# Performance work log

Measured on AMD Instinct MI355X. Metric: run time of the kernel, lower is better.

The kernel has to match this reference:

```python
import math
import jax, jax.numpy as jnp
import numpy as np

B, QC, KC, RES, SRC = 4, 512, 256, 64, 128
T = RES * RES


def setup_inputs():
    key = jax.random.key(0)
    ks = jax.random.split(key, 8)
    return {
        "key_feat": jax.random.normal(ks[0], (B, KC, SRC, SRC), jnp.float32),
        "query": jax.random.normal(ks[1], (B, QC, RES, RES), jnp.float32),
        "Weight_Mat": jax.random.uniform(ks[2], (B, T, T), dtype=jnp.float32),
        "key_proj_w": jax.random.normal(ks[3], (QC, KC), jnp.float32) * 0.02,
        "norm_w": jnp.ones((QC,), jnp.float32),
        "norm_b": jnp.zeros((QC,), jnp.float32),
        "qkv_w": jax.random.normal(ks[4], (3 * QC, 2 * QC), jnp.float32) * 0.02,
        "qkv_b": jax.random.normal(ks[5], (3 * QC,), jnp.float32) * 0.02,
        "proj_w": jax.random.normal(ks[6], (QC, QC), jnp.float32) * 0.02,
        "proj_b": jnp.zeros((QC,), jnp.float32),
    }


def group_norm(x, w, b, groups=32, eps=1e-5):
    # x: (b, C, L) -- GroupNorm over channel groups and spatial dim
    bs, C, L = x.shape
    xg = x.reshape(bs, groups, C // groups, L)
    mu = xg.mean(axis=(2, 3), keepdims=True)
    var = xg.var(axis=(2, 3), keepdims=True)
    xn = ((xg - mu) * jax.lax.rsqrt(var + eps)).reshape(bs, C, L)
    return xn * w[None, :, None] + b[None, :, None]


def reference(key_feat, query, Weight_Mat, key_proj_w, norm_w, norm_b, qkv_w, qkv_b, proj_w, proj_b):
    b, qc, H, W = query.shape
    f = key_feat.shape[2] // H  # exact integer downsample factor (2)
    # F.interpolate bilinear (align_corners=False) at exact 1/f rate == f x f average pooling
    kds = key_feat.reshape(b, key_feat.shape[1], H, f, W, f).mean(axis=(3, 5))
    # Weight_Mat interpolate has scale==1 in source (no-op), elided.
    k = jnp.einsum('oc,bchw->bohw', key_proj_w, kds).reshape(b, qc, H * W)
    q = query.reshape(b, qc, H * W)
    q = group_norm(q, norm_w, norm_b)
    k = group_norm(k, norm_w, norm_b)
    # qkv: 1x1 conv1d on concat(q, k) -> (b, 3*qc, T)
    qkv = jnp.einsum('oc,bct->bot', qkv_w, jnp.concatenate([q, k], axis=1)) + qkv_b[None, :, None]
    qq, kk, vv = jnp.split(qkv, 3, axis=1)  # each (b, qc, T); num_heads=1 so ch=qc
    scale = qc ** -0.25  # 1/sqrt(sqrt(ch))
    logits = Weight_Mat * jnp.einsum('bct,bcs->bts', qq * scale, kk * scale)
    attn = jax.nn.softmax(logits, axis=-1)
    a = jnp.einsum('bts,bcs->bct', attn, vv)
    h = jnp.einsum('oc,bct->bot', proj_w, a) + proj_b[None, :, None]
    # residual uses the NORMALIZED query, as in the source
    return (q + h).reshape(b, qc, H, W)
```

## Files before the change

kernel.cpp:

```cpp
#include <hip/hip_runtime.h>
#include <hip/hip_bf16.h>
#include <stdint.h>

#define NB 4
#define CQ 512
#define CK 256
#define TT 4096
#define SCALE_QK 0.21022410381342863f

using bf16x8 = __attribute__((ext_vector_type(8))) short;
using short4v = __attribute__((ext_vector_type(4))) short;
using f32x4  = __attribute__((ext_vector_type(4))) float;
using u32x4  = __attribute__((ext_vector_type(4))) unsigned int;
typedef unsigned short u16;

__device__ __forceinline__ u16 f2bf(float f) {
    union { float f; unsigned u; } v; v.f = f;
    return (u16)((v.u + 0x7fffu + ((v.u >> 16) & 1u)) >> 16);
}
__device__ __forceinline__ float bf2f(u16 h) {
    union { float f; unsigned u; } v; v.u = ((unsigned)h) << 16;
    return v.f;
}
__device__ __forceinline__ bf16x8 pack8(f32x4 a, f32x4 b) {
    bf16x8 r;
    r[0] = (short)f2bf(a[0]); r[1] = (short)f2bf(a[1]);
    r[2] = (short)f2bf(a[2]); r[3] = (short)f2bf(a[3]);
    r[4] = (short)f2bf(b[0]); r[5] = (short)f2bf(b[1]);
    r[6] = (short)f2bf(b[2]); r[7] = (short)f2bf(b[3]);
    return r;
}
__device__ __forceinline__ void gload_lds16(const void* g, void* l) {
    __builtin_amdgcn_global_load_lds(
        (const __attribute__((address_space(1))) unsigned int*)g,
        (__attribute__((address_space(3))) unsigned int*)l, 16, 0, 0);
}

__global__ __launch_bounds__(256) void wconv_kernel(const float* __restrict__ src,
        u16* __restrict__ dst, int n, int scale_until) {
    int i = (blockIdx.x * 256 + threadIdx.x) * 8;
    if (i >= n) return;
    f32x4 a = *(const f32x4*)(src + i);
    f32x4 c = *(const f32x4*)(src + i + 4);
    if (i < scale_until) {
        a *= SCALE_QK;
        c *= SCALE_QK;
    }
    *(bf16x8*)(dst + i) = pack8(a, c);
}

__global__ __launch_bounds__(256) void pool_tr_kernel(const float* __restrict__ kf,
                                                      u16* __restrict__ kdsT) {
    int h = blockIdx.x, b = blockIdx.y;
    __shared__ u16 tile[64][264];
    for (int idx = threadIdx.x; idx < 32 * 256; idx += 256) {
        int wp = idx & 31, c = idx >> 5;
        const float* base = kf + (((size_t)b * CK + c) * 128 + 2 * h) * 128 + 4 * wp;
        f32x4 r0 = *(const f32x4*)base;
        f32x4 r1 = *(const f32x4*)(base + 128);
        tile[2 * wp][c]     = f2bf(0.25f * (r0[0] + r0[1] + r1[0] + r1[1]));
        tile[2 * wp + 1][c] = f2bf(0.25f * (r0[2] + r0[3] + r1[2] + r1[3]));
    }
    __syncthreads();
    for (int idx = threadIdx.x; idx < 64 * 32; idx += 256) {
        int w = idx >> 5, cg = (idx & 31) << 3;
        *(u32x4*)(kdsT + ((size_t)b * TT + h * 64 + w) * CK + cg) = *(const u32x4*)&tile[w][cg];
    }
}

template <int ISBF>
__global__ __launch_bounds__(256) void gn_stats_kernel(const void* __restrict__ xv,
        const float* __restrict__ gw, const float* __restrict__ gb,
        float* __restrict__ sc, float* __restrict__ sh) {
    int g = blockIdx.x, b = blockIdx.y;
    size_t base = ((size_t)b * CQ + g * 16) * TT;
    float s = 0.f, q = 0.f;
    for (int i = threadIdx.x * 4; i < 16 * TT; i += 256 * 4) {
        float v0, v1, v2, v3;
        if constexpr (ISBF) {
            const u16* x = (const u16*)xv;
            uint2 u = *(const uint2*)(x + base + i);
            v0 = bf2f((u16)(u.x & 0xffff)); v1 = bf2f((u16)(u.x >> 16));
            v2 = bf2f((u16)(u.y & 0xffff)); v3 = bf2f((u16)(u.y >> 16));
        } else {
            const float* x = (const float*)xv;
            f32x4 v = *(const f32x4*)(x + base + i);
            v0 = v[0]; v1 = v[1]; v2 = v[2]; v3 = v[3];
        }
        s += v0 + v1 + v2 + v3;
        q += v0 * v0 + v1 * v1 + v2 * v2 + v3 * v3;
    }
#pragma unroll
    for (int d = 1; d < 64; d <<= 1) { s += __shfl_xor(s, d, 64); q += __shfl_xor(q, d, 64); }
    __shared__ float shs[4], shq[4];
    int wid = threadIdx.x >> 6;
    if ((threadIdx.x & 63) == 0) { shs[wid] = s; shq[wid] = q; }
    __syncthreads();
    if (threadIdx.x < 16) {
        float S = shs[0] + shs[1] + shs[2] + shs[3];
        float Q = shq[0] + shq[1] + shq[2] + shq[3];
        const float inv = 1.f / (16.f * TT);
        float mean = S * inv, var = Q * inv - mean * mean;
        float rstd = rsqrtf(var + 1e-5f);
        int c = g * 16 + threadIdx.x;
        float w = gw[c] * rstd;
        sc[b * CQ + c] = w;
        sh[b * CQ + c] = gb[c] - mean * w;
    }
}

template <int ISBF>
__global__ __launch_bounds__(256) void affine_tr_kernel(const void* __restrict__ xv,
        const float* __restrict__ sc, const float* __restrict__ sh, u16* __restrict__ out) {
    int t0 = blockIdx.x * 64, c0 = blockIdx.y * 64, b = blockIdx.z;
    __shared__ u16 tile[64][72];
    for (int idx = threadIdx.x; idx < 16 * 64; idx += 256) {
        int tq = idx & 15, cl = idx >> 4;
        int c = c0 + cl;
        float w = sc[b * CQ + c], z = sh[b * CQ + c];
        float v[4];
        if constexpr (ISBF) {
            short4v u = *(const short4v*)((const u16*)xv + ((size_t)b * CQ + c) * TT + t0 + 4 * tq);
#pragma unroll
            for (int j = 0; j < 4; j++) v[j] = bf2f((u16)u[j]);
        } else {
            f32x4 u = *(const f32x4*)((const float*)xv + ((size_t)b * CQ + c) * TT + t0 + 4 * tq);
#pragma unroll
            for (int j = 0; j < 4; j++) v[j] = u[j];
        }
#pragma unroll
        for (int j = 0; j < 4; j++) tile[4 * tq + j][cl] = f2bf(v[j] * w + z);
    }
    __syncthreads();
    for (int idx = threadIdx.x; idx < 64 * 8; idx += 256) {
        int tl = idx >> 3, cg = (idx & 7) << 3;
        *(u32x4*)(out + ((size_t)b * TT + t0 + tl) * CQ + c0 + cg) = *(const u32x4*)&tile[tl][cg];
    }
}

template <int EPI, int CONCAT, int SWAP>
__global__ __launch_bounds__(256) void gemm_st_kernel(
        const u16* __restrict__ Wb, const u16* __restrict__ X1, const u16* __restrict__ X2,
        int Ktot, const float* __restrict__ bias,
        u16* __restrict__ outb, u16* __restrict__ outb2, float* __restrict__ outf,
        const float* __restrict__ query, const float* __restrict__ qsc,
        const float* __restrict__ qsh) {
    int b = blockIdx.z;
    int o0 = blockIdx.x * 128, t0 = blockIdx.y * 128;
    int wid = threadIdx.x >> 6, lane = threadIdx.x & 63;
    int lr = lane & 15, lg = lane >> 4;
    int osub = (wid >> 1) * 64, tsub = (wid & 1) * 64;

    __shared__ u16 Wl[2][128][64];
    __shared__ u16 Xl[2][128][64];

    const int Kx = CONCAT ? 512 : Ktot;
    int srow = lane >> 3;
    int sxw = ((lane & 7) ^ srow) << 4;
    int xr = (lr & 7) << 4;

    f32x4 acc[4][4];
#pragma unroll
    for (int i = 0; i < 4; i++)
#pragma unroll
        for (int j = 0; j < 4; j++) acc[i][j] = f32x4{0.f, 0.f, 0.f, 0.f};

    int nk = Ktot >> 6;

#define STAGE_TILE(KC, BUF)                                                          \
    do {                                                                             \
        int c0_ = (KC) << 6;                                                         \
        const u16* xs_;                                                              \
        if (CONCAT && c0_ >= 512) xs_ = X2 + ((size_t)b * TT) * 512 + (c0_ - 512);   \
        else if (CONCAT)          xs_ = X1 + ((size_t)b * TT) * 512 + c0_;           \
        else                      xs_ = X1 + ((size_t)b * TT) * (size_t)Ktot + c0_;  \
        const char* xb_ = (const char*)(xs_ + (size_t)(t0 + wid * 32) * Kx) + sxw;   \
        const char* wb_ = (const char*)(Wb + (size_t)(o0 + wid * 32) * Ktot + c0_) + sxw; \
        _Pragma("unroll")                                                            \
        for (int i_ = 0; i_ < 4; i_++) {                                             \
            gload_lds16(xb_ + (size_t)(i_ * 8 + srow) * (Kx * 2),                    \
                        &Xl[BUF][wid * 32 + i_ * 8][0]);                             \
            gload_lds16(wb_ + (size_t)(i_ * 8 + srow) * (Ktot * 2),                  \
                        &Wl[BUF][wid * 32 + i_ * 8][0]);                             \
        }                                                                            \
    } while (0)

    STAGE_TILE(0, 0);
    __syncthreads();
    int cur = 0;
    for (int kc = 0; kc < nk; kc++) {
        if (kc + 1 < nk) STAGE_TILE(kc + 1, cur ^ 1);
#pragma unroll
        for (int kk = 0; kk < 2; kk++) {
            int boff = (kk * 64 + lg * 16) ^ xr;
            bf16x8 am[4], bn[4];
#pragma unroll
            for (int mi = 0; mi < 4; mi++) {
                if (SWAP) am[mi] = *(const bf16x8*)((const char*)&Xl[cur][tsub + mi * 16 + lr][0] + boff);
                else      am[mi] = *(const bf16x8*)((const char*)&Wl[cur][osub + mi * 16 + lr][0] + boff);
            }
#pragma unroll
            for (int ni = 0; ni < 4; ni++) {
                if (SWAP) bn[ni] = *(const bf16x8*)((const char*)&Wl[cur][osub + ni * 16 + lr][0] + boff);
                else      bn[ni] = *(const bf16x8*)((const char*)&Xl[cur][tsub + ni * 16 + lr][0] + boff);
            }
#pragma unroll
            for (int mi = 0; mi < 4; mi++)
#pragma unroll
                for (int ni = 0; ni < 4; ni++)
                    acc[mi][ni] = __builtin_amdgcn_mfma_f32_16x16x32_bf16(am[mi], bn[ni], acc[mi][ni], 0, 0, 0);
        }
        __syncthreads();
        cur ^= 1;
    }
#undef STAGE_TILE

    if (SWAP) {
#pragma unroll
        for (int mi = 0; mi < 4; mi++)
#pragma unroll
            for (int ni = 0; ni < 4; ni++)
#pragma unroll
                for (int reg = 0; reg < 4; reg++) {
                    int t = t0 + tsub + mi * 16 + 4 * lg + reg;
                    int o = o0 + osub + ni * 16 + lr;
                    float v = acc[mi][ni][reg] + bias[o] * SCALE_QK;
                    if (o < 512) outb[((size_t)b * TT + t) * 512 + o] = f2bf(v);
                    else         outb2[((size_t)b * TT + t) * 512 + (o - 512)] = f2bf(v);
                }
    } else {
#pragma unroll
        for (int mi = 0; mi < 4; mi++)
#pragma unroll
            for (int reg = 0; reg < 4; reg++) {
                int o = o0 + osub + mi * 16 + 4 * lg + reg;
                float bv = (EPI >= 1) ? bias[o] : 0.f;
#pragma unroll
                for (int ni = 0; ni < 4; ni++) {
                    int t = t0 + tsub + ni * 16 + lr;
                    size_t oidx = ((size_t)b * CQ + o) * TT + t;
                    float v = acc[mi][ni][reg] + bv;
                    if (EPI == 2) {
                        outf[oidx] = v + query[oidx] * qsc[b * CQ + o] + qsh[b * CQ + o];
                    } else {
                        outb[oidx] = f2bf(v);
                    }
                }
            }
    }
}

__global__ __launch_bounds__(512, 2) void flash_kernel(
        const u16* __restrict__ qqT, const u16* __restrict__ kkT,
        const u16* __restrict__ vv, const float* __restrict__ WM,
        u16* __restrict__ aT) {
    int b = blockIdx.y;
    int T0 = blockIdx.x * 64;
    int wid = threadIdx.x >> 6, lane = threadIdx.x & 63;
    int lr = lane & 15, lg = lane >> 4;
    int tb = wid >> 1, sb = wid & 1;

    __shared__ u16 K_lds[64][512];
    __shared__ u16 V_lds[512][64];
    __shared__ u16 p_lds[64][64];
    __shared__ float ex_max[64][2];
    __shared__ float ex_sum[64][2];

    bf16x8 qf[16];
    {
        const u16* qrow = qqT + ((size_t)b * TT + T0 + 16 * tb + lr) * CQ + lg * 8;
#pragma unroll
        for (int kc = 0; kc < 16; kc++) qf[kc] = *(const bf16x8*)(qrow + kc * 32);
    }
    f32x4 acc[16];
#pragma unroll
    for (int i = 0; i < 16; i++) acc[i] = f32x4{0.f, 0.f, 0.f, 0.f};
    float m[4], l[4];
#pragma unroll
    for (int r = 0; r < 4; r++) { m[r] = -1e30f; l[r] = 0.f; }

    const float* wmrow = WM + ((size_t)b * TT + T0 + 16 * tb + 4 * lg) * TT + 32 * sb + lr;
    const char* kbase = (const char*)(kkT + ((size_t)b * TT) * CQ);
    int myt = 16 * tb + 4 * lg;

    for (int s0 = 0; s0 < TT; s0 += 64) {
        __syncthreads();
#pragma unroll
        for (int i = 0; i < 8; i++) {
            int s = wid * 8 + i;
            gload_lds16(kbase + ((size_t)(s0 + s)) * 1024 + ((lane ^ (s & 7)) << 4),
                        &K_lds[s][0]);
        }
#pragma unroll
        for (int g2 = 0; g2 < 8; g2++) {
            int c0 = (wid * 8 + g2) * 8;
            int c = c0 + (lane >> 3);
            gload_lds16((const char*)(vv + ((size_t)b * CQ + c) * TT + s0) +
                            ((((lane & 7) ^ (c & 7))) << 4),
                        &V_lds[c0][0]);
        }
        float wmv[2][4];
#pragma unroll
        for (int fs = 0; fs < 2; fs++)
#pragma unroll
            for (int reg = 0; reg < 4; reg++)
                wmv[fs][reg] = wmrow[(size_t)reg * TT + s0 + fs * 16];
        __syncthreads();

        f32x4 sacc[2];
        sacc[0] = f32x4{0.f, 0.f, 0.f, 0.f};
        sacc[1] = f32x4{0.f, 0.f, 0.f, 0.f};
#pragma unroll
        for (int kc = 0; kc < 16; kc++) {
#pragma unroll
            for (int fs = 0; fs < 2; fs++) {
                const char* kp = (const char*)&K_lds[32 * sb + fs * 16 + lr][0];
                bf16x8 kfr = *(const bf16x8*)(kp + ((((kc << 2) | lg) ^ (lr & 7)) << 4));
                sacc[fs] = __builtin_amdgcn_mfma_f32_16x16x32_bf16(qf[kc], kfr, sacc[fs], 0, 0, 0);
            }
        }
        float lgt[2][4], pmax[4];
#pragma unroll
        for (int r = 0; r < 4; r++) pmax[r] = -3e38f;
#pragma unroll
        for (int fs = 0; fs < 2; fs++)
#pragma unroll
            for (int reg = 0; reg < 4; reg++) {
                float v = sacc[fs][reg] * wmv[fs][reg];
                lgt[fs][reg] = v;
                pmax[reg] = fmaxf(pmax[reg], v);
            }
#pragma unroll
        for (int d = 1; d < 16; d <<= 1)
#pragma unroll
            for (int reg = 0; reg < 4; reg++)
                pmax[reg] = fmaxf(pmax[reg], __shfl_xor(pmax[reg], d, 64));
        if (lr == 0) {
#pragma unroll
            for (int reg = 0; reg < 4; reg++) ex_max[myt + reg][sb] = pmax[reg];
        }
        __syncthreads();
        float fac[4], rsum[4];
#pragma unroll
        for (int reg = 0; reg < 4; reg++) {
            int t = myt + reg;
            float mn = fmaxf(m[reg], fmaxf(ex_max[t][0], ex_max[t][1]));
            fac[reg] = __expf(m[reg] - mn);
            m[reg] = mn;
            rsum[reg] = 0.f;
        }
#pragma unroll
        for (int fs = 0; fs < 2; fs++)
#pragma unroll
            for (int reg = 0; reg < 4; reg++) {
                float p = __expf(lgt[fs][reg] - m[reg]);
                rsum[reg] += p;
                int t = myt + reg;
                int s = 32 * sb + fs * 16 + lr;
                *(u16*)((char*)p_lds + t * 128 + ((((s >> 3) ^ (t & 7))) << 4) + ((s & 7) << 1)) = f2bf(p);
            }
#pragma unroll
        for (int d = 1; d < 16; d <<= 1)
#pragma unroll
            for (int reg = 0; reg < 4; reg++)
                rsum[reg] += __shfl_xor(rsum[reg], d, 64);
        if (lr == 0) {
#pragma unroll
            for (int reg = 0; reg < 4; reg++) ex_sum[myt + reg][sb] = rsum[reg];
        }
        __syncthreads();
#pragma unroll
        for (int reg = 0; reg < 4; reg++) {
            int t = myt + reg;
            l[reg] = l[reg] * fac[reg] + ex_sum[t][0] + ex_sum[t][1];
        }
#pragma unroll
        for (int nt = 0; nt < 16; nt++)
#pragma unroll
            for (int reg = 0; reg < 4; reg++) acc[nt][reg] *= fac[reg];
#pragma unroll
        for (int ks = 0; ks < 2; ks++) {
            int prow = 16 * tb + lr;
            bf16x8 pa = *(const bf16x8*)((const char*)p_lds + prow * 128 +
                                         ((((ks << 2) | lg) ^ (lr & 7)) << 4));
#pragma unroll
            for (int nt = 0; nt < 16; nt++) {
                int vr = 256 * sb + nt * 16 + lr;
                bf16x8 vf = *(const bf16x8*)((const char*)&V_lds[vr][0] +
                                             ((((ks << 2) | lg) ^ (lr & 7)) << 4));
                acc[nt] = __builtin_amdgcn_mfma_f32_16x16x32_bf16(pa, vf, acc[nt], 0, 0, 0);
            }
        }
    }
    float inv[4];
#pragma unroll
    for (int reg = 0; reg < 4; reg++) inv[reg] = 1.f / l[reg];
#pragma unroll
    for (int nt = 0; nt < 16; nt++)
#pragma unroll
        for (int reg = 0; reg < 4; reg++) {
            int t = T0 + myt + reg;
            int c = 256 * sb + nt * 16 + lr;
            aT[((size_t)b * TT + t) * CQ + c] = f2bf(acc[nt][reg] * inv[reg]);
        }
}

extern "C" void kernel_launch(void* const* d_in, const int* in_sizes, int n_in,
                              void* d_out, int out_size, void* d_ws, size_t ws_size,
                              hipStream_t stream) {
    const float* key_feat = (const float*)d_in[0];
    const float* query    = (const float*)d_in[1];
    const float* WM       = (const float*)d_in[2];
    const float* kpw      = (const float*)d_in[3];
    const float* norm_w   = (const float*)d_in[4];
    const float* norm_b   = (const float*)d_in[5];
    const float* qkv_w    = (const float*)d_in[6];
    const float* qkv_b    = (const float*)d_in[7];
    const float* proj_w   = (const float*)d_in[8];
    const float* proj_b   = (const float*)d_in[9];
    float* out = (float*)d_out;
    char* ws = (char*)d_ws;

    u16* kdsT = (u16*)(ws);
    u16* kraw = (u16*)(ws + 8388608);
    u16* qnT  = (u16*)(ws + 25165824);
    u16* knT  = (u16*)(ws + 41943040);
    u16* qqT  = (u16*)(ws + 58720256);
    u16* kkT  = (u16*)(ws + 75497472);
    u16* vvp  = (u16*)(ws + 92274688);
    u16* aT   = (u16*)(ws);
    u16* wqkv = (u16*)(ws + 16777216);
    u16* wproj= (u16*)(ws + 19922944);
    float* qsc = (float*)(ws + 109051904);
    float* qsh = qsc + NB * CQ;
    float* ksc = qsh + NB * CQ;
    float* ksh = ksc + NB * CQ;
    u16* wkp  = (u16*)(ws + 109084672);

    wconv_kernel<<<64, 256, 0, stream>>>(kpw, wkp, 512 * 256, 0);
    pool_tr_kernel<<<dim3(64, NB), 256, 0, stream>>>(key_feat, kdsT);
    gemm_st_kernel<0, 0, 0><<<dim3(4, 32, NB), 256, 0, stream>>>(
        wkp, kdsT, nullptr, CK, nullptr, kraw, nullptr, nullptr, nullptr, nullptr, nullptr);
    gn_stats_kernel<0><<<dim3(32, NB), 256, 0, stream>>>(query, norm_w, norm_b, qsc, qsh);
    gn_stats_kernel<1><<<dim3(32, NB), 256, 0, stream>>>(kraw, norm_w, norm_b, ksc, ksh);
    affine_tr_kernel<0><<<dim3(64, 8, NB), 256, 0, stream>>>(query, qsc, qsh, qnT);
    affine_tr_kernel<1><<<dim3(64, 8, NB), 256, 0, stream>>>(kraw, ksc, ksh, knT);
    wconv_kernel<<<768, 256, 0, stream>>>(qkv_w, wqkv, 1536 * 1024, 1024 * 1024);
    wconv_kernel<<<128, 256, 0, stream>>>(proj_w, wproj, 512 * 512, 0);
    gemm_st_kernel<1, 1, 1><<<dim3(8, 32, NB), 256, 0, stream>>>(
        wqkv, qnT, knT, 1024, qkv_b, qqT, kkT, nullptr, nullptr, nullptr, nullptr);
    gemm_st_kernel<1, 1, 0><<<dim3(4, 32, NB), 256, 0, stream>>>(
        wqkv + (size_t)1024 * 1024, qnT, knT, 1024, qkv_b + 1024, vvp, nullptr, nullptr,
        nullptr, nullptr, nullptr);
    flash_kernel<<<dim3(64, NB), 512, 0, stream>>>(qqT, kkT, vvp, WM, aT);
    gemm_st_kernel<2, 0, 0><<<dim3(4, 32, NB), 256, 0, stream>>>(
        wproj, aT, nullptr, CQ, proj_b, nullptr, nullptr, out, query, qsc, qsh);
}
```

Measured before the change: 542.0 us.

## Switch attention Q/K/V and probabilities to FP8 MFMA and split channels across blocks

The qkv GEMM epilogue now writes q, k and v as FP8 instead of bf16. The flash attention kernel uses fp8 MFMA for both QK^T and PV, with FP8 LDS tiles and FP8 softmax probabilities. The flash grid is also split into two channel halves per query tile, doubling the block count and raising the launch-bounds occupancy hint. This halves global/LDS traffic and uses the higher-rate fp8 matrix path, but each half recomputes the full QK^T and streams Weight_Mat twice. FP8 quantization of the probabilities and activations risks accuracy.

```diff
diff --git a/kernel.cpp b/kernel.cpp
--- a/kernel.cpp
+++ b/kernel.cpp
@@ -13,6 +13,7 @@
 using f32x4  = __attribute__((ext_vector_type(4))) float;
 using u32x4  = __attribute__((ext_vector_type(4))) unsigned int;
 typedef unsigned short u16;
+typedef uint8_t u8;
 
 __device__ __forceinline__ u16 f2bf(float f) {
     union { float f; unsigned u; } v; v.f = f;
@@ -21,6 +22,9 @@
 __device__ __forceinline__ float bf2f(u16 h) {
     union { float f; unsigned u; } v; v.u = ((unsigned)h) << 16;
     return v.f;
+}
+__device__ __forceinline__ u8 f2fp8(float f) {
+    return (u8)(__builtin_amdgcn_cvt_pk_fp8_f32(f, f, 0, false) & 0xff);
 }
 __device__ __forceinline__ bf16x8 pack8(f32x4 a, f32x4 b) {
     bf16x8 r;
@@ -142,7 +146,7 @@
 __global__ __launch_bounds__(256) void gemm_st_kernel(
         const u16* __restrict__ Wb, const u16* __restrict__ X1, const u16* __restrict__ X2,
         int Ktot, const float* __restrict__ bias,
-        u16* __restrict__ outb, u16* __restrict__ outb2, float* __restrict__ outf,
+        void* __restrict__ outb, void* __restrict__ outb2, float* __restrict__ outf,
         const float* __restrict__ query, const float* __restrict__ qsc,
         const float* __restrict__ qsh) {
     int b = blockIdx.z;
@@ -216,6 +220,8 @@
 #undef STAGE_TILE
 
     if (SWAP) {
+        u8* qq8 = (u8*)outb;
+        u8* kk8 = (u8*)outb2;
 #pragma unroll
         for (int mi = 0; mi < 4; mi++)
 #pragma unroll
@@ -225,8 +231,8 @@
                     int t = t0 + tsub + mi * 16 + 4 * lg + reg;
                     int o = o0 + osub + ni * 16 + lr;
                     float v = acc[mi][ni][reg] + bias[o] * SCALE_QK;
-                    if (o < 512) outb[((size_t)b * TT + t) * 512 + o] = f2bf(v);
-                    else         outb2[((size_t)b * TT + t) * 512 + (o - 512)] = f2bf(v);
+                    if (o < 512) qq8[((size_t)b * TT + t) * 512 + o] = f2fp8(v);
+                    else         kk8[((size_t)b * TT + t) * 512 + (o - 512)] = f2fp8(v);
                 }
     } else {
 #pragma unroll
@@ -242,61 +248,65 @@
                     float v = acc[mi][ni][reg] + bv;
                     if (EPI == 2) {
                         outf[oidx] = v + query[oidx] * qsc[b * CQ + o] + qsh[b * CQ + o];
+                    } else if (EPI == 1) {
+                        ((u8*)outb)[oidx] = f2fp8(v);
                     } else {
-                        outb[oidx] = f2bf(v);
+                        ((u16*)outb)[oidx] = f2bf(v);
                     }
                 }
             }
     }
 }
 
-__global__ __launch_bounds__(512, 2) void flash_kernel(
-        const u16* __restrict__ qqT, const u16* __restrict__ kkT,
-        const u16* __restrict__ vv, const float* __restrict__ WM,
+__global__ __launch_bounds__(512, 4) void flash_kernel(
+        const u8* __restrict__ qq8, const u8* __restrict__ kk8,
+        const u8* __restrict__ vv8, const float* __restrict__ WM,
         u16* __restrict__ aT) {
-    int b = blockIdx.y;
-    int T0 = blockIdx.x * 64;
+    int chalf = blockIdx.x;
+    int T0 = blockIdx.y * 64;
+    int b = blockIdx.z;
     int wid = threadIdx.x >> 6, lane = threadIdx.x & 63;
     int lr = lane & 15, lg = lane >> 4;
-    int tb = wid >> 1, sb = wid & 1;
-
-    __shared__ u16 K_lds[64][512];
-    __shared__ u16 V_lds[512][64];
-    __shared__ u16 p_lds[64][64];
+    int tb = wid >> 1, cb = wid & 1;
+
+    __shared__ u8 K_lds[64][512];
+    __shared__ u8 V_lds[256][64];
+    __shared__ u8 p_lds[64][64];
     __shared__ float ex_max[64][2];
     __shared__ float ex_sum[64][2];
 
-    bf16x8 qf[16];
+    long qf[16];
     {
-        const u16* qrow = qqT + ((size_t)b * TT + T0 + 16 * tb + lr) * CQ + lg * 8;
-#pragma unroll
-        for (int kc = 0; kc < 16; kc++) qf[kc] = *(const bf16x8*)(qrow + kc * 32);
-    }
-    f32x4 acc[16];
-#pragma unroll
-    for (int i = 0; i < 16; i++) acc[i] = f32x4{0.f, 0.f, 0.f, 0.f};
+        const u8* qrow = qq8 + ((size_t)b * TT + T0 + 16 * tb + lr) * 512 + lg * 8;
+#pragma unroll
+        for (int kc = 0; kc < 16; kc++) qf[kc] = *(const long*)(qrow + kc * 32);
+    }
+    f32x4 acc[8];
+#pragma unroll
+    for (int i = 0; i < 8; i++) acc[i] = f32x4{0.f, 0.f, 0.f, 0.f};
     float m[4], l[4];
 #pragma unroll
     for (int r = 0; r < 4; r++) { m[r] = -1e30f; l[r] = 0.f; }
 
-    const float* wmrow = WM + ((size_t)b * TT + T0 + 16 * tb + 4 * lg) * TT + 32 * sb + lr;
-    const char* kbase = (const char*)(kkT + ((size_t)b * TT) * CQ);
+    const float* wmrow = WM + ((size_t)b * TT + T0 + 16 * tb + 4 * lg) * TT + 32 * cb + lr;
+    const u8* kbase = kk8 + (size_t)b * TT * 512;
+    const u8* vbase = vv8 + ((size_t)b * CQ + chalf * 256) * TT;
     int myt = 16 * tb + 4 * lg;
 
     for (int s0 = 0; s0 < TT; s0 += 64) {
         __syncthreads();
 #pragma unroll
-        for (int i = 0; i < 8; i++) {
-            int s = wid * 8 + i;
-            gload_lds16(kbase + ((size_t)(s0 + s)) * 1024 + ((lane ^ (s & 7)) << 4),
-                        &K_lds[s][0]);
-        }
-#pragma unroll
-        for (int g2 = 0; g2 < 8; g2++) {
-            int c0 = (wid * 8 + g2) * 8;
-            int c = c0 + (lane >> 3);
-            gload_lds16((const char*)(vv + ((size_t)b * CQ + c) * TT + s0) +
-                            ((((lane & 7) ^ (c & 7))) << 4),
+        for (int i = 0; i < 4; i++) {
+            int r0 = wid * 8 + i * 2;
+            int s = r0 + (lane >> 5);
+            gload_lds16(kbase + (size_t)(s0 + s) * 512 + (((lane & 31) ^ (s & 7)) << 4),
+                        &K_lds[r0][0]);
+        }
+#pragma unroll
+        for (int i = 0; i < 2; i++) {
+            int c0 = wid * 32 + i * 16;
+            int c = c0 + (lane >> 2);
+            gload_lds16(vbase + (size_t)c * TT + s0 + (((lane & 3) ^ (c & 3)) << 4),
                         &V_lds[c0][0]);
         }
         float wmv[2][4];
@@ -314,9 +324,10 @@
         for (int kc = 0; kc < 16; kc++) {
 #pragma unroll
             for (int fs = 0; fs < 2; fs++) {
-                const char* kp = (const char*)&K_lds[32 * sb + fs * 16 + lr][0];
-                bf16x8 kfr = *(const bf16x8*)(kp + ((((kc << 2) | lg) ^ (lr & 7)) << 4));
-                sacc[fs] = __builtin_amdgcn_mfma_f32_16x16x32_bf16(qf[kc], kfr, sacc[fs], 0, 0, 0);
+                int srow = 32 * cb + fs * 16 + lr;
+                long kfr = *(const long*)(&K_lds[srow][0] +
+                            ((((kc << 1) | (lg >> 1)) ^ (srow & 7)) << 4) + ((lg & 1) << 3));
+                sacc[fs] = __builtin_amdgcn_mfma_f32_16x16x32_fp8_fp8(qf[kc], kfr, sacc[fs], 0, 0, 0);
             }
         }
         float lgt[2][4], pmax[4];
@@ -337,7 +348,7 @@
                 pmax[reg] = fmaxf(pmax[reg], __shfl_xor(pmax[reg], d, 64));
         if (lr == 0) {
 #pragma unroll
-            for (int reg = 0; reg < 4; reg++) ex_max[myt + reg][sb] = pmax[reg];
+            for (int reg = 0; reg < 4; reg++) ex_max[myt + reg][cb] = pmax[reg];
         }
         __syncthreads();
         float fac[4], rsum[4];
@@ -356,8 +367,7 @@
                 float p = __expf(lgt[fs][reg] - m[reg]);
                 rsum[reg] += p;
                 int t = myt + reg;
-                int s = 32 * sb + fs * 16 + lr;
-                *(u16*)((char*)p_lds + t * 128 + ((((s >> 3) ^ (t & 7))) << 4) + ((s & 7) << 1)) = f2bf(p);
+                p_lds[t][((((cb << 1) | fs) ^ (t & 3)) << 4) + lr] = f2fp8(p);
             }
 #pragma unroll
         for (int d = 1; d < 16; d <<= 1)
@@ -366,7 +376,7 @@
                 rsum[reg] += __shfl_xor(rsum[reg], d, 64);
         if (lr == 0) {
 #pragma unroll
-            for (int reg = 0; reg < 4; reg++) ex_sum[myt + reg][sb] = rsum[reg];
+            for (int reg = 0; reg < 4; reg++) ex_sum[myt + reg][cb] = rsum[reg];
         }
         __syncthreads();
 #pragma unroll
@@ -375,20 +385,20 @@
             l[reg] = l[reg] * fac[reg] + ex_sum[t][0] + ex_sum[t][1];
         }
 #pragma unroll
-        for (int nt = 0; nt < 16; nt++)
-#pragma unroll
-            for (int reg = 0; reg < 4; reg++) acc[nt][reg] *= fac[reg];
+        for (int nc = 0; nc < 8; nc++)
+#pragma unroll
+            for (int reg = 0; reg < 4; reg++) acc[nc][reg] *= fac[reg];
 #pragma unroll
         for (int ks = 0; ks < 2; ks++) {
             int prow = 16 * tb + lr;
-            bf16x8 pa = *(const bf16x8*)((const char*)p_lds + prow * 128 +
-                                         ((((ks << 2) | lg) ^ (lr & 7)) << 4));
-#pragma unroll
-            for (int nt = 0; nt < 16; nt++) {
-                int vr = 256 * sb + nt * 16 + lr;
-                bf16x8 vf = *(const bf16x8*)((const char*)&V_lds[vr][0] +
-                                             ((((ks << 2) | lg) ^ (lr & 7)) << 4));
-                acc[nt] = __builtin_amdgcn_mfma_f32_16x16x32_bf16(pa, vf, acc[nt], 0, 0, 0);
+            long pa = *(const long*)(&p_lds[prow][0] +
+                        ((((ks << 1) | (lg >> 1)) ^ (prow & 3)) << 4) + ((lg & 1) << 3));
+#pragma unroll
+            for (int nc = 0; nc < 8; nc++) {
+                int vr = cb * 128 + nc * 16 + lr;
+                long vf = *(const long*)(&V_lds[vr][0] +
+                            ((((ks << 1) | (lg >> 1)) ^ (vr & 3)) << 4) + ((lg & 1) << 3));
+                acc[nc] = __builtin_amdgcn_mfma_f32_16x16x32_fp8_fp8(pa, vf, acc[nc], 0, 0, 0);
             }
         }
     }
@@ -396,12 +406,12 @@
 #pragma unroll
     for (int reg = 0; reg < 4; reg++) inv[reg] = 1.f / l[reg];
 #pragma unroll
-    for (int nt = 0; nt < 16; nt++)
+    for (int nc = 0; nc < 8; nc++)
 #pragma unroll
         for (int reg = 0; reg < 4; reg++) {
             int t = T0 + myt + reg;
-            int c = 256 * sb + nt * 16 + lr;
-            aT[((size_t)b * TT + t) * CQ + c] = f2bf(acc[nt][reg] * inv[reg]);
+            int c = chalf * 256 + cb * 128 + nc * 16 + lr;
+            aT[((size_t)b * TT + t) * CQ + c] = f2bf(acc[nc][reg] * inv[reg]);
         }
 }
 
@@ -425,9 +435,9 @@
     u16* kraw = (u16*)(ws + 8388608);
     u16* qnT  = (u16*)(ws + 25165824);
     u16* knT  = (u16*)(ws + 41943040);
-    u16* qqT  = (u16*)(ws + 58720256);
-    u16* kkT  = (u16*)(ws + 75497472);
-    u16* vvp  = (u16*)(ws + 92274688);
+    u8*  qq8  = (u8*)(ws + 58720256);
+    u8*  kk8  = (u8*)(ws + 67108864);
+    u8*  vv8  = (u8*)(ws + 75497472);
     u16* aT   = (u16*)(ws);
     u16* wqkv = (u16*)(ws + 16777216);
     u16* wproj= (u16*)(ws + 19922944);
@@ -448,11 +458,11 @@
     wconv_kernel<<<768, 256, 0, stream>>>(qkv_w, wqkv, 1536 * 1024, 1024 * 1024);
     wconv_kernel<<<128, 256, 0, stream>>>(proj_w, wproj, 512 * 512, 0);
     gemm_st_kernel<1, 1, 1><<<dim3(8, 32, NB), 256, 0, stream>>>(
-        wqkv, qnT, knT, 1024, qkv_b, qqT, kkT, nullptr, nullptr, nullptr, nullptr);
+        wqkv, qnT, knT, 1024, qkv_b, qq8, kk8, nullptr, nullptr, nullptr, nullptr);
     gemm_st_kernel<1, 1, 0><<<dim3(4, 32, NB), 256, 0, stream>>>(
-        wqkv + (size_t)1024 * 1024, qnT, knT, 1024, qkv_b + 1024, vvp, nullptr, nullptr,
-        nullptr, nullptr, nullptr);
-    flash_kernel<<<dim3(64, NB), 512, 0, stream>>>(qqT, kkT, vvp, WM, aT);
+        wqkv + (size_t)1024 * 1024, qnT, knT, 1024, qkv_b + 1024, vv8, nullptr,
+        nullptr, nullptr, nullptr, nullptr);
+    flash_kernel<<<dim3(2, 64, NB), 512, 0, stream>>>(qq8, kk8, vv8, WM, aT);
     gemm_st_kernel<2, 0, 0><<<dim3(4, 32, NB), 256, 0, stream>>>(
         wproj, aT, nullptr, CQ, proj_b, nullptr, nullptr, out, query, qsc, qsh);
 }
```

After: 749.5 us. +38.3%, slower.
